# Optimization experiments

Measured on AMD Instinct MI355X. Metric: run time of the kernel, lower is better.

Reference implementation:

```python
import jax, jax.numpy as jnp
import numpy as np

C = 1.0        # curvature parameter (manifold curvature -1/C)
EPS = 1e-7


def expmap0_space(v, k):
    # v: [..., ds] spatial tangent vector at the hyperboloid origin (time comp 0)
    # returns ambient point [..., ds+1] = (sqrt(k)cosh(|v|/sqrt(k)), sqrt(k)sinh(|v|/sqrt(k)) v/|v|)
    sk = jnp.sqrt(k)
    n = jnp.maximum(jnp.linalg.norm(v, axis=-1, keepdims=True), EPS)
    t = sk * jnp.cosh(n / sk)
    s = sk * jnp.sinh(n / sk) * (v / n)
    return jnp.concatenate([t, s], axis=-1)


def logmap0_space(p, k):
    # p: [..., ds+1] hyperboloid point -> spatial tangent [..., ds] at origin
    sk = jnp.sqrt(k)
    t, s = p[..., :1], p[..., 1:]
    ns = jnp.maximum(jnp.linalg.norm(s, axis=-1, keepdims=True), EPS)
    d = sk * jnp.arccosh(jnp.maximum(t / sk, 1.0 + EPS))
    return d * (s / ns)


def setup_inputs() -> dict:
    key = jax.random.key(0)
    N, DS, E = 50000, 127, 800000
    ks = jax.random.split(key, 8)
    x = jax.random.normal(ks[0], (N, DS), dtype=jnp.float32) * 0.1
    edge_src = jax.random.randint(ks[1], (E,), 0, N)
    edge_dst = jax.random.randint(ks[2], (E,), 0, N)
    edge_weight = jax.random.uniform(ks[3], (E,), dtype=jnp.float32) / 16.0  # ~1/deg norm
    sc = 1.0 / np.sqrt(DS)
    W1 = jax.random.normal(ks[4], (DS, DS), dtype=jnp.float32) * sc
    b1 = jnp.zeros((DS,), dtype=jnp.float32)
    W2 = jax.random.normal(ks[5], (DS, DS), dtype=jnp.float32) * sc
    b2 = jnp.zeros((DS,), dtype=jnp.float32)
    return {"x": x, "W1": W1, "b1": b1, "W2": W2, "b2": b2,
            "edge_src": edge_src, "edge_dst": edge_dst, "edge_weight": edge_weight}


def reference(x, W1, b1, W2, b2, edge_src, edge_dst, edge_weight):
    N = x.shape[0]
    # encode(): cat zero time column + expmap0 onto hyperboloid
    p = expmap0_space(x, C)                 # [N, ds+1]
    h = logmap0_space(p, C)                 # tangent features at origin [N, ds]
    for (W, b) in ((W1, b1), (W2, b2)):
        # hyperbolic linear in tangent space
        z = h @ W + b                       # [N, ds]
        # adjacency-based neighbor aggregation (sparse spmm via edge list)
        msg = edge_weight[:, None] * z[edge_src]          # [E, ds] irregular gather
        agg = jax.ops.segment_sum(msg, edge_dst, num_segments=N)
        # activation + skip connection, back onto the manifold between layers
        h = jax.nn.relu(agg) + h
        h = logmap0_space(expmap0_space(h, C), C)
    return expmap0_space(h, C)              # [N, ds+1] on hyperboloid
```

## Files before the change

### kernel.cpp

```cpp
#include <hip/hip_runtime.h>

#define EPS 1e-7f
#define DS 127
#define DP 128
#define NBMAX 512
#define CAP 4096
#define CH 2048

typedef short bf16x8 __attribute__((ext_vector_type(8)));
typedef float f32x4  __attribute__((ext_vector_type(4)));
typedef float f32x2  __attribute__((ext_vector_type(2)));

__device__ __forceinline__ float wave_sum(float v) {
#pragma unroll
    for (int off = 32; off > 0; off >>= 1)
        v += __shfl_xor(v, off, 64);
    return v;
}

__device__ __forceinline__ unsigned short f2bf(float f) {
    unsigned u = __float_as_uint(f);
    unsigned r = (u + 0x7FFFu + ((u >> 16) & 1u)) >> 16;
    return (unsigned short)r;
}

__device__ __forceinline__ unsigned pack_bf2(float a, float b) {
    return (unsigned)f2bf(a) | ((unsigned)f2bf(b) << 16);
}

__device__ __forceinline__ unsigned char f2fp8(float v) {
    return (unsigned char)(__builtin_amdgcn_cvt_pk_fp8_f32(v, v, 0, false) & 0xFF);
}

__device__ __forceinline__ float logexp_scale(float n2) {
    float nrm = sqrtf(n2);
    return (nrm >= 4.472136e-4f) ? 1.0f : (4.472136e-4f / fmaxf(nrm, EPS));
}

__device__ __forceinline__ void sinhcosh(float n, float& sh, float& ch) {
    float e  = __expf(n);
    float em = __expf(-n);
    sh = 0.5f * (e - em);
    ch = 0.5f * (e + em);
}

__global__ void f_first_kernel(const float* __restrict__ x,
                               unsigned* __restrict__ hbu, int N) {
    int gw   = (int)((blockIdx.x * blockDim.x + threadIdx.x) >> 6);
    int lane = threadIdx.x & 63;
    if (gw >= N) return;

    const float* row = x + (size_t)gw * DS;
    float x0 = row[2 * lane];
    float x1 = (lane < 63) ? row[2 * lane + 1] : 0.f;

    float scale = logexp_scale(wave_sum(x0 * x0 + x1 * x1));
    hbu[(size_t)gw * (DP / 2) + lane] = pack_bf2(scale * x0,
                                                 (lane < 63) ? scale * x1 : 0.f);
}

__global__ void padT_kernel(const float* __restrict__ W1, const float* __restrict__ b1,
                            unsigned short* __restrict__ Wt1, float* __restrict__ bp1,
                            const float* __restrict__ W2, const float* __restrict__ b2,
                            unsigned short* __restrict__ Wt2, float* __restrict__ bp2) {
    const float* W = blockIdx.y ? W2 : W1;
    const float* b = blockIdx.y ? b2 : b1;
    unsigned short* Wt = blockIdx.y ? Wt2 : Wt1;
    float* bp = blockIdx.y ? bp2 : bp1;
    int i = blockIdx.x * blockDim.x + threadIdx.x;
    if (i < DP * DP) {
        int n = i >> 7, k = i & (DP - 1);
        Wt[i] = (k < DS && n < DS) ? f2bf(W[k * DS + n]) : (unsigned short)0;
    } else if (i < DP * DP + DP) {
        int j = i - DP * DP;
        bp[j] = (j < DS) ? b[j] : 0.f;
    }
}

#define BM 64
__global__ __launch_bounds__(256) void gemm_mfma_kernel(
        const unsigned short* __restrict__ hb,
        const unsigned short* __restrict__ Wt,
        const float* __restrict__ bp,
        unsigned char* __restrict__ z8, int N) {
    int wave = threadIdx.x >> 6;
    int lane = threadIdx.x & 63;
    int m    = lane & 15;
    int quad = lane >> 4;
    int r0   = blockIdx.x * BM + wave * 16;

    f32x4 acc[8];
#pragma unroll
    for (int t = 0; t < 8; t++) acc[t] = (f32x4){0.f, 0.f, 0.f, 0.f};

    const bf16x8* arow = (const bf16x8*)(hb + (size_t)(r0 + m) * DP);
#pragma unroll
    for (int kq = 0; kq < 4; kq++) {
        bf16x8 a = arow[kq * 4 + quad];
#pragma unroll
        for (int nt = 0; nt < 8; nt++) {
            bf16x8 bfr = ((const bf16x8*)(Wt + (size_t)(nt * 16 + m) * DP))[kq * 4 + quad];
            acc[nt] = __builtin_amdgcn_mfma_f32_16x16x32_bf16(a, bfr, acc[nt], 0, 0, 0);
        }
    }

#pragma unroll
    for (int nt = 0; nt < 8; nt++) {
        float bias = bp[nt * 16 + m];
#pragma unroll
        for (int reg = 0; reg < 4; reg++) {
            int row = r0 + quad * 4 + reg;
            if (row < N)
                z8[(size_t)row * DP + nt * 16 + m] = f2fp8(acc[nt][reg] + bias);
        }
    }
}

__global__ __launch_bounds__(256) void binA_kernel(
        const int* __restrict__ es, const int* __restrict__ ed,
        const float* __restrict__ ew,
        int* __restrict__ gcnt, unsigned* __restrict__ stg_pk,
        unsigned char* __restrict__ stg_r, int E) {
    __shared__ int  lcnt[NBMAX];
    __shared__ int  loff[NBMAX];
    __shared__ int  gbase[NBMAX];
    __shared__ unsigned       lst_pk[CH];
    __shared__ unsigned short lst_d[CH];

    int tid  = threadIdx.x;
    int lane = tid & 63;
    int base = blockIdx.x * CH;
    int cnt  = min(CH, E - base);

    for (int b = tid; b < NBMAX; b += 256) lcnt[b] = 0;
    __syncthreads();

    unsigned pk[CH / 256];
    int      rd[CH / 256];
#pragma unroll
    for (int k = 0; k < CH / 256; k++) {
        int i = base + k * 256 + tid;
        if (i < E) {
            int d = ed[i];
            rd[k] = d;
            pk[k] = ((unsigned)f2bf(ew[i]) << 16) | (unsigned)es[i];
            atomicAdd(&lcnt[d >> 7], 1);
        } else {
            rd[k] = -1;
        }
    }
    __syncthreads();

    if (tid < 64) {
        int carry = 0;
        for (int c = 0; c < NBMAX; c += 64) {
            int v = lcnt[c + lane];
            int inc = v;
#pragma unroll
            for (int off = 1; off < 64; off <<= 1) {
                int t = __shfl_up(inc, off, 64);
                if (lane >= off) inc += t;
            }
            loff[c + lane] = carry + inc - v;
            carry += __shfl(inc, 63, 64);
        }
    }
    __syncthreads();
    for (int b = tid; b < NBMAX; b += 256) lcnt[b] = 0;
    __syncthreads();

#pragma unroll
    for (int k = 0; k < CH / 256; k++) {
        if (rd[k] >= 0) {
            int b = rd[k] >> 7;
            int slot = loff[b] + atomicAdd(&lcnt[b], 1);
            lst_pk[slot] = pk[k];
            lst_d[slot]  = (unsigned short)rd[k];
        }
    }
    __syncthreads();

    for (int b = tid; b < NBMAX; b += 256) {
        int c = lcnt[b];
        gbase[b] = c ? atomicAdd(&gcnt[b], c) : 0;
    }
    __syncthreads();

    for (int s = tid; s < cnt; s += 256) {
        unsigned p = lst_pk[s];
        int d = lst_d[s];
        int b = d >> 7;
        int idx = gbase[b] + (s - loff[b]);
        if (idx >= CAP) idx = CAP - 1;
        stg_pk[(size_t)b * CAP + idx] = p;
        stg_r [(size_t)b * CAP + idx] = (unsigned char)(d & 127);
    }
}

__global__ void bscan_kernel(const int* __restrict__ gcnt, int nb,
                             int* __restrict__ bstart,
                             int* __restrict__ row_start, int N, int E) {
    int lane = threadIdx.x;
    int base = 0;
    for (int c = 0; c < nb; c += 64) {
        int idx = c + lane;
        int v = (idx < nb) ? min(gcnt[idx], CAP) : 0;
        int inc = v;
#pragma unroll
        for (int off = 1; off < 64; off <<= 1) {
            int t = __shfl_up(inc, off, 64);
            if (lane >= off) inc += t;
        }
        if (idx < nb) bstart[idx] = base + inc - v;
        base += __shfl(inc, 63, 64);
    }
    if (lane == 0) row_start[N] = E;
}

__global__ __launch_bounds__(256) void binB_kernel(
        const unsigned* __restrict__ stg_pk, const unsigned char* __restrict__ stg_r,
        const int* __restrict__ gcnt, const int* __restrict__ bstart,
        int* __restrict__ row_start, unsigned* __restrict__ epk, int N) {
    __shared__ int rcnt[128];
    __shared__ int roff[128];

    int b    = blockIdx.x;
    int tid  = threadIdx.x;
    int lane = tid & 63;
    int cnt  = min(gcnt[b], CAP);
    int bb   = bstart[b];
    const unsigned*      in_pk = stg_pk + (size_t)b * CAP;
    const unsigned char* in_r  = stg_r  + (size_t)b * CAP;

    if (tid < 128) rcnt[tid] = 0;
    __syncthreads();

    for (int i = tid; i < cnt; i += 256)
        atomicAdd(&rcnt[in_r[i]], 1);
    __syncthreads();

    if (tid < 64) {
        int carry = 0;
        for (int c = 0; c < 128; c += 64) {
            int v = rcnt[c + lane];
            int inc = v;
#pragma unroll
            for (int off = 1; off < 64; off <<= 1) {
                int t = __shfl_up(inc, off, 64);
                if (lane >= off) inc += t;
            }
            roff[c + lane] = carry + inc - v;
            carry += __shfl(inc, 63, 64);
        }
    }
    __syncthreads();

    if (tid < 128) {
        int row = b * 128 + tid;
        if (row < N) row_start[row] = bb + roff[tid];
        rcnt[tid] = 0;
    }
    __syncthreads();

    for (int i = tid; i < cnt; i += 256) {
        int r = in_r[i];
        int pos = atomicAdd(&rcnt[r], 1);
        epk[bb + roff[r] + pos] = in_pk[i];
    }
}

#define GATHER(K)                                                             \
    {                                                                         \
        unsigned pks[K], us[K];                                               \
        _Pragma("unroll")                                                     \
        for (int i = 0; i < K; i++) pks[i] = epk[e + i];                      \
        _Pragma("unroll")                                                     \
        for (int i = 0; i < K; i++)                                           \
            us[i] = *(const unsigned short*)(zc + (((pks[i] & 0xFFFFu) << 7) + lane2)); \
        _Pragma("unroll")                                                     \
        for (int i = 0; i < K; i++) {                                         \
            float wf = __uint_as_float(pks[i] & 0xFFFF0000u);                 \
            f32x2 zv = __builtin_amdgcn_cvt_pk_f32_fp8(us[i], false);         \
            a0 = fmaf(wf, zv.x, a0);                                          \
            a1 = fmaf(wf, zv.y, a1);                                          \
        }                                                                     \
    }

template <bool LAST>
__global__ void agg_f_tpl(const unsigned char* __restrict__ zc,
                          const unsigned* __restrict__ hbu_in,
                          const int* __restrict__ row_start,
                          const unsigned* __restrict__ epk,
                          unsigned* __restrict__ hbu_out,
                          float* __restrict__ out, int N) {
    int gw   = (int)((blockIdx.x * blockDim.x + threadIdx.x) >> 6);
    int lane = threadIdx.x & 63;
    if (gw >= N) return;
    gw = __builtin_amdgcn_readfirstlane(gw);
    int lane2 = lane << 1;

    int beg = row_start[gw], end = row_start[gw + 1];
    float a0 = 0.f, a1 = 0.f;

    int e = beg;
    for (; e + 16 <= end; e += 16) GATHER(16)
    for (; e + 8 <= end; e += 8)  GATHER(8)
    if (e < end) {
        int last = end - 1;
        unsigned pks[8], us[8];
#pragma unroll
        for (int i = 0; i < 8; i++) {
            int ei = e + i;
            unsigned p = epk[ei > last ? last : ei];
            if (ei > last) p &= 0xFFFFu;
            pks[i] = p;
        }
#pragma unroll
        for (int i = 0; i < 8; i++)
            us[i] = *(const unsigned short*)(zc + (((pks[i] & 0xFFFFu) << 7) + lane2));
#pragma unroll
        for (int i = 0; i < 8; i++) {
            float wf = __uint_as_float(pks[i] & 0xFFFF0000u);
            f32x2 zv = __builtin_amdgcn_cvt_pk_f32_fp8(us[i], false);
            a0 = fmaf(wf, zv.x, a0);
            a1 = fmaf(wf, zv.y, a1);
        }
    }

    unsigned hu = hbu_in[(size_t)gw * (DP / 2) + lane];
    float x0 = __uint_as_float(hu << 16) + fmaxf(a0, 0.f);
    float x1 = (lane < 63) ? __uint_as_float(hu & 0xFFFF0000u) + fmaxf(a1, 0.f)
                           : 0.f;

    float n2 = wave_sum(x0 * x0 + x1 * x1);
    float scale = logexp_scale(n2);
    float y0 = scale * x0;
    float y1 = (lane < 63) ? scale * x1 : 0.f;

    if (!LAST) {
        hbu_out[(size_t)gw * (DP / 2) + lane] = pack_bf2(y0, y1);
    } else {
        float n2y = scale * scale * n2;
        float ny  = fmaxf(sqrtf(n2y), EPS);
        float shy, chy;
        sinhcosh(ny, shy, chy);
        float sc  = shy / ny;
        float* orow = out + (size_t)gw * DP;
        if (lane == 0) orow[0] = chy;
        orow[1 + 2 * lane] = sc * y0;
        if (lane < 63) orow[2 + 2 * lane] = sc * y1;
    }
}

extern "C" void kernel_launch(void* const* d_in, const int* in_sizes, int n_in,
                              void* d_out, int out_size, void* d_ws, size_t ws_size,
                              hipStream_t stream) {
    const float* x  = (const float*)d_in[0];
    const float* W1 = (const float*)d_in[1];
    const float* b1 = (const float*)d_in[2];
    const float* W2 = (const float*)d_in[3];
    const float* b2 = (const float*)d_in[4];
    const int*   es = (const int*)d_in[5];
    const int*   ed = (const int*)d_in[6];
    const float* ew = (const float*)d_in[7];

    const int N  = in_sizes[0] / DS;
    const int E  = in_sizes[5];
    const int NR = (N + BM - 1) / BM * BM;
    const int NB = (N + 127) >> 7;

    unsigned short* hb  = (unsigned short*)d_ws;
    unsigned char*  z8  = (unsigned char*)(hb + (size_t)NR * DP);
    unsigned short* Wt1 = (unsigned short*)(z8 + (size_t)N * DP);
    unsigned short* Wt2 = Wt1 + DP * DP;
    float* bp1          = (float*)(Wt2 + DP * DP);
    float* bp2          = bp1 + DP;
    unsigned* epk       = (unsigned*)(bp2 + DP);
    int*   row_start    = (int*)(epk + E);
    int*   gcnt         = row_start + N + 1;
    int*   bstart       = gcnt + NBMAX;
    unsigned* stg_pk    = (unsigned*)(bstart + NBMAX);
    unsigned char* stg_r = (unsigned char*)(stg_pk + (size_t)NBMAX * CAP);

    unsigned* hbu = (unsigned*)hb;

    const int fBlocks    = (N * 64 + 255) / 256;
    const int gemmBlocks = (N + BM - 1) / BM;
    const int padBlocks  = (DP * DP + DP + 255) / 256;
    const int binABlocks = (E + CH - 1) / CH;

    hipMemsetAsync(gcnt, 0, NBMAX * sizeof(int), stream);
    binA_kernel<<<binABlocks, 256, 0, stream>>>(es, ed, ew, gcnt, stg_pk, stg_r, E);
    bscan_kernel<<<1, 64, 0, stream>>>(gcnt, NB, bstart, row_start, N, E);
    binB_kernel<<<NB, 256, 0, stream>>>(stg_pk, stg_r, gcnt, bstart,
                                        row_start, epk, N);

    padT_kernel<<<dim3(padBlocks, 2), 256, 0, stream>>>(W1, b1, Wt1, bp1,
                                                        W2, b2, Wt2, bp2);

    f_first_kernel<<<fBlocks, 256, 0, stream>>>(x, hbu, N);

    gemm_mfma_kernel<<<gemmBlocks, 256, 0, stream>>>(hb, Wt1, bp1, z8, N);
    agg_f_tpl<false><<<fBlocks, 256, 0, stream>>>(z8, hbu, row_start, epk,
                                                  hbu, nullptr, N);

    gemm_mfma_kernel<<<gemmBlocks, 256, 0, stream>>>(hb, Wt2, bp2, z8, N);
    agg_f_tpl<true><<<fBlocks, 256, 0, stream>>>(z8, hbu, row_start, epk,
                                                 nullptr, (float*)d_out, N);
}
```

Baseline: 236.3 us.

## Merge prep launches, fold bucket scan into binB, and tighten gather tail

The memset, weight pad/transpose and first feature-normalisation kernels are fused into one prep kernel. The single-block bucket scan kernel is removed: each binB block now computes its own prefix offset by summing earlier bucket counts in one wave, while the other three waves build the row histogram. The aggregation tail replaces the masked 8-wide fallback with 8/4/2/1 power-of-two gathers. The aim is fewer launches and serial gaps, at the cost of redundant prefix sums across blocks and fewer threads for the histogram.

```diff
diff --git a/kernel.cpp b/kernel.cpp
--- a/kernel.cpp
+++ b/kernel.cpp
@@ -6,12 +6,20 @@
 #define NBMAX 512
 #define CAP 4096
 #define CH 2048
+#define PADB ((DP * DP + DP + 255) / 256)
 
 typedef short bf16x8 __attribute__((ext_vector_type(8)));
 typedef float f32x4  __attribute__((ext_vector_type(4)));
 typedef float f32x2  __attribute__((ext_vector_type(2)));
 
 __device__ __forceinline__ float wave_sum(float v) {
+#pragma unroll
+    for (int off = 32; off > 0; off >>= 1)
+        v += __shfl_xor(v, off, 64);
+    return v;
+}
+
+__device__ __forceinline__ int wave_sum_i(int v) {
 #pragma unroll
     for (int off = 32; off > 0; off >>= 1)
         v += __shfl_xor(v, off, 64);
@@ -44,10 +52,43 @@
     ch = 0.5f * (e + em);
 }
 
-__global__ void f_first_kernel(const float* __restrict__ x,
-                               unsigned* __restrict__ hbu, int N) {
-    int gw   = (int)((blockIdx.x * blockDim.x + threadIdx.x) >> 6);
-    int lane = threadIdx.x & 63;
+__global__ __launch_bounds__(256) void prep_kernel(
+        const float* __restrict__ x, unsigned* __restrict__ hbu, int N,
+        const float* __restrict__ W1, const float* __restrict__ b1,
+        unsigned short* __restrict__ Wt1, float* __restrict__ bp1,
+        const float* __restrict__ W2, const float* __restrict__ b2,
+        unsigned short* __restrict__ Wt2, float* __restrict__ bp2,
+        int* __restrict__ gcnt) {
+    int bid = blockIdx.x;
+    int tid = threadIdx.x;
+
+    if (bid == 0) {
+        for (int i = tid; i < NBMAX; i += 256) gcnt[i] = 0;
+        return;
+    }
+    bid -= 1;
+
+    if (bid < 2 * PADB) {
+        int layer = (bid >= PADB);
+        int pb    = bid - layer * PADB;
+        const float* W = layer ? W2 : W1;
+        const float* b = layer ? b2 : b1;
+        unsigned short* Wt = layer ? Wt2 : Wt1;
+        float* bp = layer ? bp2 : bp1;
+        int i = pb * 256 + tid;
+        if (i < DP * DP) {
+            int n = i >> 7, k = i & (DP - 1);
+            Wt[i] = (k < DS && n < DS) ? f2bf(W[k * DS + n]) : (unsigned short)0;
+        } else if (i < DP * DP + DP) {
+            int j = i - DP * DP;
+            bp[j] = (j < DS) ? b[j] : 0.f;
+        }
+        return;
+    }
+    bid -= 2 * PADB;
+
+    int gw   = bid * 4 + (tid >> 6);
+    int lane = tid & 63;
     if (gw >= N) return;
 
     const float* row = x + (size_t)gw * DS;
@@ -57,24 +98,6 @@
     float scale = logexp_scale(wave_sum(x0 * x0 + x1 * x1));
     hbu[(size_t)gw * (DP / 2) + lane] = pack_bf2(scale * x0,
                                                  (lane < 63) ? scale * x1 : 0.f);
-}
-
-__global__ void padT_kernel(const float* __restrict__ W1, const float* __restrict__ b1,
-                            unsigned short* __restrict__ Wt1, float* __restrict__ bp1,
-                            const float* __restrict__ W2, const float* __restrict__ b2,
-                            unsigned short* __restrict__ Wt2, float* __restrict__ bp2) {
-    const float* W = blockIdx.y ? W2 : W1;
-    const float* b = blockIdx.y ? b2 : b1;
-    unsigned short* Wt = blockIdx.y ? Wt2 : Wt1;
-    float* bp = blockIdx.y ? bp2 : bp1;
-    int i = blockIdx.x * blockDim.x + threadIdx.x;
-    if (i < DP * DP) {
-        int n = i >> 7, k = i & (DP - 1);
-        Wt[i] = (k < DS && n < DS) ? f2bf(W[k * DS + n]) : (unsigned short)0;
-    } else if (i < DP * DP + DP) {
-        int j = i - DP * DP;
-        bp[j] = (j < DS) ? b[j] : 0.f;
-    }
 }
 
 #define BM 64
@@ -197,47 +220,38 @@
     }
 }
 
-__global__ void bscan_kernel(const int* __restrict__ gcnt, int nb,
-                             int* __restrict__ bstart,
-                             int* __restrict__ row_start, int N, int E) {
-    int lane = threadIdx.x;
-    int base = 0;
-    for (int c = 0; c < nb; c += 64) {
-        int idx = c + lane;
-        int v = (idx < nb) ? min(gcnt[idx], CAP) : 0;
-        int inc = v;
-#pragma unroll
-        for (int off = 1; off < 64; off <<= 1) {
-            int t = __shfl_up(inc, off, 64);
-            if (lane >= off) inc += t;
-        }
-        if (idx < nb) bstart[idx] = base + inc - v;
-        base += __shfl(inc, 63, 64);
-    }
-    if (lane == 0) row_start[N] = E;
-}
-
 __global__ __launch_bounds__(256) void binB_kernel(
         const unsigned* __restrict__ stg_pk, const unsigned char* __restrict__ stg_r,
-        const int* __restrict__ gcnt, const int* __restrict__ bstart,
-        int* __restrict__ row_start, unsigned* __restrict__ epk, int N) {
+        const int* __restrict__ gcnt,
+        int* __restrict__ row_start, unsigned* __restrict__ epk,
+        int N, int E) {
     __shared__ int rcnt[128];
     __shared__ int roff[128];
+    __shared__ int sh_bb;
 
     int b    = blockIdx.x;
     int tid  = threadIdx.x;
     int lane = tid & 63;
+    int wave = tid >> 6;
     int cnt  = min(gcnt[b], CAP);
-    int bb   = bstart[b];
     const unsigned*      in_pk = stg_pk + (size_t)b * CAP;
     const unsigned char* in_r  = stg_r  + (size_t)b * CAP;
 
     if (tid < 128) rcnt[tid] = 0;
-    __syncthreads();
-
-    for (int i = tid; i < cnt; i += 256)
-        atomicAdd(&rcnt[in_r[i]], 1);
-    __syncthreads();
+    if (b == 0 && tid == 0) row_start[N] = E;
+    __syncthreads();
+
+    if (wave == 3) {
+        int acc = 0;
+        for (int c = lane; c < b; c += 64) acc += min(gcnt[c], CAP);
+        acc = wave_sum_i(acc);
+        if (lane == 0) sh_bb = acc;
+    } else {
+        for (int i = tid; i < cnt; i += 192)
+            atomicAdd(&rcnt[in_r[i]], 1);
+    }
+    __syncthreads();
+    int bb = sh_bb;
 
     if (tid < 64) {
         int carry = 0;
@@ -304,28 +318,10 @@
 
     int e = beg;
     for (; e + 16 <= end; e += 16) GATHER(16)
-    for (; e + 8 <= end; e += 8)  GATHER(8)
-    if (e < end) {
-        int last = end - 1;
-        unsigned pks[8], us[8];
-#pragma unroll
-        for (int i = 0; i < 8; i++) {
-            int ei = e + i;
-            unsigned p = epk[ei > last ? last : ei];
-            if (ei > last) p &= 0xFFFFu;
-            pks[i] = p;
-        }
-#pragma unroll
-        for (int i = 0; i < 8; i++)
-            us[i] = *(const unsigned short*)(zc + (((pks[i] & 0xFFFFu) << 7) + lane2));
-#pragma unroll
-        for (int i = 0; i < 8; i++) {
-            float wf = __uint_as_float(pks[i] & 0xFFFF0000u);
-            f32x2 zv = __builtin_amdgcn_cvt_pk_f32_fp8(us[i], false);
-            a0 = fmaf(wf, zv.x, a0);
-            a1 = fmaf(wf, zv.y, a1);
-        }
-    }
+    if (e + 8 <= end) { GATHER(8) e += 8; }
+    if (e + 4 <= end) { GATHER(4) e += 4; }
+    if (e + 2 <= end) { GATHER(2) e += 2; }
+    if (e < end)      { GATHER(1) }
 
     unsigned hu = hbu_in[(size_t)gw * (DP / 2) + lane];
     float x0 = __uint_as_float(hu << 16) + fmaxf(a0, 0.f);
@@ -378,27 +374,22 @@
     unsigned* epk       = (unsigned*)(bp2 + DP);
     int*   row_start    = (int*)(epk + E);
     int*   gcnt         = row_start + N + 1;
-    int*   bstart       = gcnt + NBMAX;
-    unsigned* stg_pk    = (unsigned*)(bstart + NBMAX);
+    unsigned* stg_pk    = (unsigned*)(gcnt + NBMAX);
     unsigned char* stg_r = (unsigned char*)(stg_pk + (size_t)NBMAX * CAP);
 
     unsigned* hbu = (unsigned*)hb;
 
     const int fBlocks    = (N * 64 + 255) / 256;
     const int gemmBlocks = (N + BM - 1) / BM;
-    const int padBlocks  = (DP * DP + DP + 255) / 256;
     const int binABlocks = (E + CH - 1) / CH;
-
-    hipMemsetAsync(gcnt, 0, NBMAX * sizeof(int), stream);
+    const int prepBlocks = 1 + 2 * PADB + fBlocks;
+
+    prep_kernel<<<prepBlocks, 256, 0, stream>>>(x, hbu, N,
+                                                W1, b1, Wt1, bp1,
+                                                W2, b2, Wt2, bp2, gcnt);
+
     binA_kernel<<<binABlocks, 256, 0, stream>>>(es, ed, ew, gcnt, stg_pk, stg_r, E);
-    bscan_kernel<<<1, 64, 0, stream>>>(gcnt, NB, bstart, row_start, N, E);
-    binB_kernel<<<NB, 256, 0, stream>>>(stg_pk, stg_r, gcnt, bstart,
-                                        row_start, epk, N);
-
-    padT_kernel<<<dim3(padBlocks, 2), 256, 0, stream>>>(W1, b1, Wt1, bp1,
-                                                        W2, b2, Wt2, bp2);
-
-    f_first_kernel<<<fBlocks, 256, 0, stream>>>(x, hbu, N);
+    binB_kernel<<<NB, 256, 0, stream>>>(stg_pk, stg_r, gcnt, row_start, epk, N, E);
 
     gemm_mfma_kernel<<<gemmBlocks, 256, 0, stream>>>(hb, Wt1, bp1, z8, N);
     agg_f_tpl<false><<<fBlocks, 256, 0, stream>>>(z8, hbu, row_start, epk,
```

New measurement: 221.1 us. 6.4% less time.
